# Kernel optimization log

Measured on AMD Instinct MI355X. Metric: run time of the kernel, lower is better.

The kernel has to match this reference:

```python
import jax, jax.numpy as jnp
import numpy as np

IN_F, OUT_F, RANK = 4096, 4096, 1024
B, S_LEN = 4, 2048


def _dequant(data, scale, zp):
    # (int_data - zero_point) * scale, per-tensor scalar quantization
    return (data.astype(jnp.float32) - zp.astype(jnp.float32)) * scale.astype(jnp.float32)


def setup_inputs() -> dict:
    key = jax.random.key(0)
    ks = jax.random.split(key, 8)
    x = jax.random.normal(ks[0], (B, S_LEN, IN_F), dtype=jnp.float32)
    U_data = jax.random.randint(ks[1], (OUT_F, RANK), 0, 255, dtype=jnp.int32)
    S_data = jax.random.randint(ks[2], (RANK,), 0, 255, dtype=jnp.int32)
    Vh_data = jax.random.randint(ks[3], (RANK, IN_F), 0, 255, dtype=jnp.int32)
    bias = jax.random.normal(ks[4], (OUT_F,), dtype=jnp.float32)
    return {
        "x": x,
        "U_data": U_data,
        "U_scale": jnp.array([0.02], dtype=jnp.float32),
        "U_zp": jnp.array([128.0], dtype=jnp.float32),
        "S_data": S_data,
        "S_scale": jnp.array([0.05], dtype=jnp.float32),
        "S_zp": jnp.array([128.0], dtype=jnp.float32),
        "Vh_data": Vh_data,
        "Vh_scale": jnp.array([0.02], dtype=jnp.float32),
        "Vh_zp": jnp.array([128.0], dtype=jnp.float32),
        "bias": bias,
    }


def reference(x, U_data, U_scale, U_zp, S_data, S_scale, S_zp,
              Vh_data, Vh_scale, Vh_zp, bias):
    U = _dequant(U_data, U_scale, U_zp)     # [out, r]
    S = _dequant(S_data, S_scale, S_zp)     # [r]
    Vh = _dequant(Vh_data, Vh_scale, Vh_zp)  # [r, in]
    orig_shape = x.shape
    x_flat = x.reshape(-1, orig_shape[-1])  # [N, in]
    h = x_flat @ Vh.T                        # [N, r]
    h = h * S[None, :]
    y = h @ U.T                              # [N, out]
    y = y + bias
    return y.reshape(orig_shape[:-1] + (U.shape[0],))
```

## Files before the change

kernel.cpp:

```cpp
#include <hip/hip_runtime.h>
#include <stdint.h>

#define NROWS 8192
#define INF   4096
#define OUTF  4096
#define RNK   1024

typedef unsigned short u16;
typedef __attribute__((ext_vector_type(8))) short bf16x8;
typedef __attribute__((ext_vector_type(4))) float f32x4;
typedef __attribute__((ext_vector_type(8))) unsigned short u16x8;

__device__ __forceinline__ u16 f32_bf16(float f) {
  union { float f; uint32_t u; } v; v.f = f;
  return (u16)((v.u + 0x7FFF + ((v.u >> 16) & 1)) >> 16);
}


__global__ __launch_bounds__(256) void convert_x(const float* __restrict__ x,
                                                 u16* __restrict__ o) {
  int t = blockIdx.x * 256 + threadIdx.x;
  int e = t * 8;
  float4 a = *(const float4*)(x + e);
  float4 b = *(const float4*)(x + e + 4);
  u16x8 r;
  r[0] = f32_bf16(a.x); r[1] = f32_bf16(a.y); r[2] = f32_bf16(a.z); r[3] = f32_bf16(a.w);
  r[4] = f32_bf16(b.x); r[5] = f32_bf16(b.y); r[6] = f32_bf16(b.z); r[7] = f32_bf16(b.w);
  *(u16x8*)(o + e) = r;
}

__global__ __launch_bounds__(256) void dequant_vh(const int* __restrict__ vh,
                                                  const float* __restrict__ vs,
                                                  const float* __restrict__ vz,
                                                  const int* __restrict__ sd,
                                                  const float* __restrict__ ss,
                                                  const float* __restrict__ sz,
                                                  u16* __restrict__ o) {
  int t = blockIdx.x * 256 + threadIdx.x;
  int e = t * 4;
  int row = e >> 12;
  float sval = ((float)sd[row] - sz[0]) * ss[0];
  float sc = vs[0] * sval;
  float zp = vz[0];
  int4 d = *(const int4*)(vh + e);
  ushort4 r;
  r.x = f32_bf16(((float)d.x - zp) * sc);
  r.y = f32_bf16(((float)d.y - zp) * sc);
  r.z = f32_bf16(((float)d.z - zp) * sc);
  r.w = f32_bf16(((float)d.w - zp) * sc);
  *(ushort4*)(o + e) = r;
}

__global__ __launch_bounds__(256) void dequant_u(const int* __restrict__ ud,
                                                 const float* __restrict__ us,
                                                 const float* __restrict__ uz,
                                                 u16* __restrict__ o) {
  int t = blockIdx.x * 256 + threadIdx.x;
  int e = t * 4;
  float sc = us[0];
  float zp = uz[0];
  int4 d = *(const int4*)(ud + e);
  ushort4 r;
  r.x = f32_bf16(((float)d.x - zp) * sc);
  r.y = f32_bf16(((float)d.y - zp) * sc);
  r.z = f32_bf16(((float)d.z - zp) * sc);
  r.w = f32_bf16(((float)d.w - zp) * sc);
  *(ushort4*)(o + e) = r;
}


__device__ __forceinline__ void gl_lds16(const u16* g, u16* l) {
  __builtin_amdgcn_global_load_lds(
      (const __attribute__((address_space(1))) void*)g,
      (__attribute__((address_space(3))) void*)l, 16, 0, 0);
}

template <int VM> __device__ __forceinline__ void vm_wait() {
  static_assert(VM == 3 || VM == 4, "unexpected vmcnt");
  if constexpr (VM == 3) asm volatile("s_waitcnt vmcnt(3)" ::: "memory");
  if constexpr (VM == 4) asm volatile("s_waitcnt vmcnt(4)" ::: "memory");
}

template <int BN, int WM, int WN, int K, int N, bool OUT_BF16, bool ADD_BIAS>
__global__ __launch_bounds__(512, 2) void gemm2b(const u16* __restrict__ A,
                                                 const u16* __restrict__ B,
                                                 void* __restrict__ Cv,
                                                 const float* __restrict__ bias) {
  constexpr int BM = 256, BK = 64;
  constexpr int AR = 128 / WM;
  constexpr int BC = (BN / 2) / WN;
  constexpr int AI = AR / 16;
  constexpr int BJ = BC / 16;
  constexpr int LB = (BN == 256) ? 2 : 1;
  constexpr int NT = K / BK;
  constexpr int AH = 128 * BK;
  constexpr int BH = (BN / 2) * BK;

  constexpr int NXB = N / BN;
  constexpr int NYB = NROWS / BM;
  constexpr int NWG = NXB * NYB;
  static_assert(NWG % 8 == 0, "XCD swizzle requires nwg % 8 == 0");
  constexpr int CPX = NWG / 8;

  __shared__ __attribute__((aligned(16))) u16 ldsA[2 * 2 * AH];
  __shared__ __attribute__((aligned(16))) u16 ldsB[2 * 2 * BH];

  const int tid  = threadIdx.x;
  const int lane = tid & 63;
  const int wave = tid >> 6;
  const int wn   = wave % WN;
  const int wm   = wave / WN;

  const int L    = blockIdx.y * NXB + blockIdx.x;
  const int orig = (L & 7) * CPX + (L >> 3);
  const int bm   = (orig / NXB) * BM;
  const int bn   = (orig % NXB) * BN;

  const int srow = tid >> 3;
  const int spc  = tid & 7;
  const int sgc  = spc ^ (srow & 7);

  const u16* gA = A + (size_t)(bm + srow) * K + sgc * 8;
  const u16* gB = B + (size_t)(bn + srow) * K + sgc * 8;
  u16* lA = ldsA + srow * BK + spc * 8;
  u16* lB = ldsB + srow * BK + spc * 8;

#define STAGE_A(buf, h, kt)                                                    \
  { const u16* g_ = gA + (size_t)(h) * 128 * K + (kt);                         \
    u16* l_ = lA + ((buf) * 2 + (h)) * AH;                                     \
    gl_lds16(g_, l_);                                                          \
    gl_lds16(g_ + (size_t)64 * K, l_ + 64 * BK); }

#define STAGE_B(buf, h, kt)                                                    \
  { const u16* g_ = gB + (size_t)(h) * (BN / 2) * K + (kt);                    \
    u16* l_ = lB + ((buf) * 2 + (h)) * BH;                                     \
    gl_lds16(g_, l_);                                                          \
    if constexpr (LB == 2) gl_lds16(g_ + (size_t)64 * K, l_ + 64 * BK); }

  const int r   = lane & 15;
  const int kq  = (lane >> 4) * 8;
  const int pc0 = (((kq) >> 3) ^ (r & 7)) << 3;
  const int pc1 = (((32 + kq) >> 3) ^ (r & 7)) << 3;

  f32x4 acc[2][2][AI][BJ] = {};
  bf16x8 af[AI][2];
  bf16x8 bf0[BJ][2];
  bf16x8 bf1[BJ][2];

#define LOAD_A(buf, ih)                                                        \
  { const u16* ab = ldsA + ((buf) * 2 + (ih)) * AH + (wm * AR + r) * BK;       \
    _Pragma("unroll")                                                          \
    for (int i = 0; i < AI; ++i) {                                             \
      af[i][0] = *(const bf16x8*)(ab + i * 16 * BK + pc0);                     \
      af[i][1] = *(const bf16x8*)(ab + i * 16 * BK + pc1);                     \
    } }

#define LOAD_B(dst, buf, jh)                                                   \
  { const u16* bb = ldsB + ((buf) * 2 + (jh)) * BH + (wn * BC + r) * BK;       \
    _Pragma("unroll")                                                          \
    for (int j = 0; j < BJ; ++j) {                                             \
      dst[j][0] = *(const bf16x8*)(bb + j * 16 * BK + pc0);                    \
      dst[j][1] = *(const bf16x8*)(bb + j * 16 * BK + pc1);                    \
    } }

#define MFMA_Q(ih, jh, bsrc)                                                   \
  _Pragma("unroll")                                                            \
  for (int i = 0; i < AI; ++i)                                                 \
    _Pragma("unroll")                                                          \
    for (int j = 0; j < BJ; ++j) {                                             \
      acc[ih][jh][i][j] = __builtin_amdgcn_mfma_f32_16x16x32_bf16(             \
          af[i][0], bsrc[j][0], acc[ih][jh][i][j], 0, 0, 0);                   \
      acc[ih][jh][i][j] = __builtin_amdgcn_mfma_f32_16x16x32_bf16(             \
          af[i][1], bsrc[j][1], acc[ih][jh][i][j], 0, 0, 0);                   \
    }

#define SB  __builtin_amdgcn_sched_barrier(0)
#define BAR __builtin_amdgcn_s_barrier()
#define PRIO1 __builtin_amdgcn_s_setprio(1)
#define PRIO0 __builtin_amdgcn_s_setprio(0)

  STAGE_A(0, 0, 0);
  STAGE_B(0, 0, 0);
  STAGE_B(0, 1, 0);
  STAGE_A(0, 1, 0);
  SB;
  constexpr int KT1 = (NT > 1 ? BK : 0);
  STAGE_A(1, 0, KT1);
  STAGE_B(1, 1, KT1);
  SB;
  vm_wait<2 + LB>();
  BAR; SB;

  for (int t = 0; t < NT; ++t) {
    const int buf  = t & 1;
    const int nbuf = buf ^ 1;
    const int kt1 = (t + 1 < NT ? t + 1 : NT - 1) * BK;
    const int kt2 = (t + 2 < NT ? t + 2 : NT - 1) * BK;

    LOAD_A(buf, 0);
    LOAD_B(bf0, buf, 0);
    LOAD_B(bf1, buf, 1);
    STAGE_A(nbuf, 1, kt1);
    STAGE_B(nbuf, 0, kt1);
    SB;
    PRIO1; MFMA_Q(0, 0, bf0); PRIO0;
    PRIO1; MFMA_Q(0, 1, bf1); PRIO0;
    SB; BAR; SB;

    STAGE_A(buf, 0, kt2);
    STAGE_B(buf, 1, kt2);
    SB;
    LOAD_A(buf, 1);
    PRIO1; MFMA_Q(1, 1, bf1); PRIO0;
    PRIO1; MFMA_Q(1, 0, bf0); PRIO0;
    SB;
    vm_wait<2 + LB>();
    BAR; SB;
  }

  const int col0 = lane & 15;
  const int row0 = (lane >> 4) * 4;
#pragma unroll
  for (int ih = 0; ih < 2; ++ih)
#pragma unroll
    for (int jh = 0; jh < 2; ++jh)
#pragma unroll
      for (int j = 0; j < BJ; ++j) {
        const int gcol = bn + jh * (BN / 2) + wn * BC + j * 16 + col0;
        float bv = 0.f;
        if constexpr (ADD_BIAS) bv = bias[gcol];
#pragma unroll
        for (int i = 0; i < AI; ++i)
#pragma unroll
          for (int rr = 0; rr < 4; ++rr) {
            const int grow = bm + ih * 128 + wm * AR + i * 16 + row0 + rr;
            float v = acc[ih][jh][i][j][rr] + bv;
            if constexpr (OUT_BF16)
              ((u16*)Cv)[(size_t)grow * N + gcol] = f32_bf16(v);
            else
              ((float*)Cv)[(size_t)grow * N + gcol] = v;
          }
      }
#undef MFMA_Q
#undef LOAD_A
#undef LOAD_B
#undef STAGE_A
#undef STAGE_B
#undef SB
#undef BAR
#undef PRIO1
#undef PRIO0
}


extern "C" void kernel_launch(void* const* d_in, const int* in_sizes, int n_in,
                              void* d_out, int out_size, void* d_ws, size_t ws_size,
                              hipStream_t stream) {
  const float* x        = (const float*)d_in[0];
  const int*   U_data   = (const int*)d_in[1];
  const float* U_scale  = (const float*)d_in[2];
  const float* U_zp     = (const float*)d_in[3];
  const int*   S_data   = (const int*)d_in[4];
  const float* S_scale  = (const float*)d_in[5];
  const float* S_zp     = (const float*)d_in[6];
  const int*   Vh_data  = (const int*)d_in[7];
  const float* Vh_scale = (const float*)d_in[8];
  const float* Vh_zp    = (const float*)d_in[9];
  const float* bias     = (const float*)d_in[10];
  float* out = (float*)d_out;

  char* ws = (char*)d_ws;
  u16* xb  = (u16*)ws;
  u16* vhb = (u16*)(ws + (size_t)67108864);
  u16* ub  = (u16*)(ws + (size_t)67108864 + 8388608);
  u16* hb  = (u16*)(ws + (size_t)67108864 + 16777216);

  convert_x<<<NROWS * INF / (8 * 256), 256, 0, stream>>>(x, xb);
  dequant_vh<<<RNK * INF / (4 * 256), 256, 0, stream>>>(Vh_data, Vh_scale, Vh_zp,
                                                        S_data, S_scale, S_zp, vhb);
  dequant_u<<<OUTF * RNK / (4 * 256), 256, 0, stream>>>(U_data, U_scale, U_zp, ub);

  gemm2b<128, 4, 2, INF, RNK, true, false>
      <<<dim3(RNK / 128, NROWS / 256), 512, 0, stream>>>(xb, vhb, (void*)hb, nullptr);

  gemm2b<256, 2, 4, RNK, OUTF, false, true>
      <<<dim3(OUTF / 256, NROWS / 256), 512, 0, stream>>>(hb, ub, (void*)out, bias);
}
```

Before: 420.9 us.

## Restructure GEMM main loop into four barrier-separated MFMA phases with deeper prefetch

```diff
diff --git a/kernel.cpp b/kernel.cpp
--- a/kernel.cpp
+++ b/kernel.cpp
@@ -76,16 +76,16 @@
 }
 
 template <int VM> __device__ __forceinline__ void vm_wait() {
-  static_assert(VM == 3 || VM == 4, "unexpected vmcnt");
-  if constexpr (VM == 3) asm volatile("s_waitcnt vmcnt(3)" ::: "memory");
-  if constexpr (VM == 4) asm volatile("s_waitcnt vmcnt(4)" ::: "memory");
+  static_assert(VM == 5 || VM == 6, "unexpected vmcnt");
+  if constexpr (VM == 5) asm volatile("s_waitcnt vmcnt(5)" ::: "memory");
+  if constexpr (VM == 6) asm volatile("s_waitcnt vmcnt(6)" ::: "memory");
 }
 
 template <int BN, int WM, int WN, int K, int N, bool OUT_BF16, bool ADD_BIAS>
-__global__ __launch_bounds__(512, 2) void gemm2b(const u16* __restrict__ A,
-                                                 const u16* __restrict__ B,
-                                                 void* __restrict__ Cv,
-                                                 const float* __restrict__ bias) {
+__global__ __launch_bounds__(512, 2) void gemm5(const u16* __restrict__ A,
+                                                const u16* __restrict__ B,
+                                                void* __restrict__ Cv,
+                                                const float* __restrict__ bias) {
   constexpr int BM = 256, BK = 64;
   constexpr int AR = 128 / WM;
   constexpr int BC = (BN / 2) / WN;
@@ -95,6 +95,7 @@
   constexpr int NT = K / BK;
   constexpr int AH = 128 * BK;
   constexpr int BH = (BN / 2) * BK;
+  constexpr int VMN = 4 + LB;
 
   constexpr int NXB = N / BN;
   constexpr int NYB = NROWS / BM;
@@ -174,8 +175,8 @@
           af[i][1], bsrc[j][1], acc[ih][jh][i][j], 0, 0, 0);                   \
     }
 
-#define SB  __builtin_amdgcn_sched_barrier(0)
-#define BAR __builtin_amdgcn_s_barrier()
+#define BAR   __builtin_amdgcn_s_barrier()
+#define LGKM0 asm volatile("s_waitcnt lgkmcnt(0)" ::: "memory")
 #define PRIO1 __builtin_amdgcn_s_setprio(1)
 #define PRIO0 __builtin_amdgcn_s_setprio(0)
 
@@ -183,13 +184,12 @@
   STAGE_B(0, 0, 0);
   STAGE_B(0, 1, 0);
   STAGE_A(0, 1, 0);
-  SB;
   constexpr int KT1 = (NT > 1 ? BK : 0);
   STAGE_A(1, 0, KT1);
   STAGE_B(1, 1, KT1);
-  SB;
-  vm_wait<2 + LB>();
-  BAR; SB;
+  STAGE_A(1, 1, KT1);
+  vm_wait<VMN>();
+  BAR;
 
   for (int t = 0; t < NT; ++t) {
     const int buf  = t & 1;
@@ -199,23 +199,30 @@
 
     LOAD_A(buf, 0);
     LOAD_B(bf0, buf, 0);
+    STAGE_B(nbuf, 0, kt1);
+    if constexpr (AI * 2 + BJ * 2 >= 12)
+      asm volatile("s_waitcnt lgkmcnt(8)" ::: "memory");
+    BAR; LGKM0;
+    PRIO1; MFMA_Q(0, 0, bf0); PRIO0;
+    BAR;
+
     LOAD_B(bf1, buf, 1);
-    STAGE_A(nbuf, 1, kt1);
-    STAGE_B(nbuf, 0, kt1);
-    SB;
-    PRIO1; MFMA_Q(0, 0, bf0); PRIO0;
+    STAGE_A(buf, 0, kt2);
+    BAR; LGKM0;
     PRIO1; MFMA_Q(0, 1, bf1); PRIO0;
-    SB; BAR; SB;
-
-    STAGE_A(buf, 0, kt2);
+    BAR;
+
+    LOAD_A(buf, 1);
     STAGE_B(buf, 1, kt2);
-    SB;
-    LOAD_A(buf, 1);
+    BAR; LGKM0;
     PRIO1; MFMA_Q(1, 1, bf1); PRIO0;
+    BAR;
+
+    STAGE_A(buf, 1, kt2);
+    BAR;
     PRIO1; MFMA_Q(1, 0, bf0); PRIO0;
-    SB;
-    vm_wait<2 + LB>();
-    BAR; SB;
+    vm_wait<VMN>();
+    BAR;
   }
 
   const int col0 = lane & 15;
@@ -246,8 +253,8 @@
 #undef LOAD_B
 #undef STAGE_A
 #undef STAGE_B
-#undef SB
 #undef BAR
+#undef LGKM0
 #undef PRIO1
 #undef PRIO0
 }
@@ -280,9 +287,9 @@
                                                         S_data, S_scale, S_zp, vhb);
   dequant_u<<<OUTF * RNK / (4 * 256), 256, 0, stream>>>(U_data, U_scale, U_zp, ub);
 
-  gemm2b<128, 4, 2, INF, RNK, true, false>
+  gemm5<128, 4, 2, INF, RNK, true, false>
       <<<dim3(RNK / 128, NROWS / 256), 512, 0, stream>>>(xb, vhb, (void*)hb, nullptr);
 
-  gemm2b<256, 2, 4, RNK, OUTF, false, true>
+  gemm5<256, 2, 4, RNK, OUTF, false, true>
       <<<dim3(OUTF / 256, NROWS / 256), 512, 0, stream>>>(hb, ub, (void*)out, bias);
 }
```

New measurement: 453.5 us. 1.08x slower.
